# Performance work log

Measured on AMD Instinct MI355X. Metric: run time of the kernel, lower is better.

## Reference

```python
import jax, jax.numpy as jnp
import numpy as np

N_USERS = 100_000
N_ITEMS = 200_000
N_EDGES = 1_000_000
D = 64        # in_size == every layer_size
L = 3         # number of NGCF layers
B = 4096      # BPR batch
SLOPE = 0.2   # LeakyReLU negative slope
EPS = 1e-12   # F.normalize eps


def setup_inputs() -> dict:
    key = jax.random.key(0)
    ks = jax.random.split(key, 11)
    s = 1.0 / np.sqrt(D)  # xavier-ish scale
    return dict(
        user_feat=jax.random.normal(ks[0], (N_USERS, D), jnp.float32) * s,
        item_feat=jax.random.normal(ks[1], (N_ITEMS, D), jnp.float32) * s,
        W1=jax.random.normal(ks[2], (L, D, D), jnp.float32) * s,
        b1=jnp.zeros((L, D), jnp.float32),
        W2=jax.random.normal(ks[3], (L, D, D), jnp.float32) * s,
        b2=jnp.zeros((L, D), jnp.float32),
        edge_src=jax.random.randint(ks[4], (N_EDGES,), 0, N_USERS),
        edge_dst=jax.random.randint(ks[5], (N_EDGES,), 0, N_ITEMS),
        users=jax.random.randint(ks[6], (B,), 0, N_USERS),
        pos_items=jax.random.randint(ks[7], (B,), 0, N_ITEMS),
        neg_items=jax.random.randint(ks[8], (B,), 0, N_ITEMS),
    )


def _act_norm(h):
    # LeakyReLU(0.2) -> (dropout=identity, eval) -> row-wise L2 normalize
    h = jax.nn.leaky_relu(h, SLOPE)
    n = jnp.linalg.norm(h, axis=1, keepdims=True)
    return h / jnp.maximum(n, EPS)


def _ngcf_forward(user_feat, item_feat, W1, b1, W2, b2, edge_src, edge_dst):
    ones = jnp.ones((edge_src.shape[0],), user_feat.dtype)
    deg_u = jax.ops.segment_sum(ones, edge_src, num_segments=N_USERS)  # out-degree of users
    deg_i = jax.ops.segment_sum(ones, edge_dst, num_segments=N_ITEMS)  # in-degree of items
    norm = (deg_u[edge_src] * deg_i[edge_dst]) ** -0.5  # [E], same for both directions
    norm = norm[:, None]

    hu, hi = user_feat, item_feat
    u_embeds, i_embeds = [hu], [hi]
    for l in range(L):
        # per-edge elementwise product term (shared between both directions)
        p = hu[edge_src] * hi[edge_dst]            # [E, D]
        pw = p @ W2[l] + b2[l]                     # [E, D]
        # user -> item messages, summed per item
        m_i = norm * ((hu @ W1[l] + b1[l])[edge_src] + pw)
        # item -> user messages, summed per user
        m_u = norm * ((hi @ W1[l] + b1[l])[edge_dst] + pw)
        hi_new = jax.ops.segment_sum(m_i, edge_dst, num_segments=N_ITEMS)
        hu_new = jax.ops.segment_sum(m_u, edge_src, num_segments=N_USERS)
        hu, hi = _act_norm(hu_new), _act_norm(hi_new)
        u_embeds.append(hu)
        i_embeds.append(hi)

    user_embd = jnp.concatenate(u_embeds, axis=1)  # [N_USERS, D*(L+1)]
    item_embd = jnp.concatenate(i_embeds, axis=1)  # [N_ITEMS, D*(L+1)]
    return user_embd, item_embd


def reference(user_feat, item_feat, W1, b1, W2, b2,
              edge_src, edge_dst, users, pos_items, neg_items):
    user_embd, item_embd = _ngcf_forward(
        user_feat, item_feat, W1, b1, W2, b2, edge_src, edge_dst)
    return (user_embd[users], item_embd[pos_items], item_embd[neg_items])
```

## Files before the change

kernel.cpp:

```cpp
#include <hip/hip_runtime.h>

#define NU 100000
#define NI 200000
#define NE 1000000
#define NB 4096
#define CAP 16384
#define NBS 98
#define NBD 98
#define NTI (NI / 16)
#define NTU (NU / 16)

typedef __attribute__((ext_vector_type(8))) short bf16x8;
typedef __attribute__((ext_vector_type(4))) float f32x4;
typedef __attribute__((ext_vector_type(8))) unsigned short u16x8;

static __device__ __forceinline__ short f2bf(float f) {
  unsigned u = __builtin_bit_cast(unsigned, f);
  unsigned r = (u + 0x7fffu + ((u >> 16) & 1u)) >> 16;
  return (short)r;
}
static __device__ __forceinline__ float bf2f(unsigned short u) {
  return __builtin_bit_cast(float, ((unsigned)u) << 16);
}

__global__ __launch_bounds__(256) void binA_kernel(const int* __restrict__ src,
                                                   const int* __restrict__ dst,
                                                   int* __restrict__ gcur_s,
                                                   int* __restrict__ gcur_d,
                                                   int2* __restrict__ temp_s,
                                                   int2* __restrict__ temp_d) {
  __shared__ int lh[128], lbase[128], lpos[128];
  const int dir = blockIdx.x >> 9;
  const int cb = blockIdx.x & 511;
  const int lo = (int)(((long long)NE * cb) >> 9);
  const int hi = (int)(((long long)NE * (cb + 1)) >> 9);
  const int* key = dir ? dst : src;
  const int* oth = dir ? src : dst;
  int* gcur = dir ? gcur_d : gcur_s;
  int2* temp = dir ? temp_d : temp_s;
  const int shift = dir ? 11 : 10;
  const int tid = threadIdx.x;
  if (tid < 128) lh[tid] = 0;
  __syncthreads();
  for (int e = lo + tid; e < hi; e += 256) atomicAdd(&lh[key[e] >> shift], 1);
  __syncthreads();
  if (tid < 128) {
    const int c = lh[tid];
    lbase[tid] = c ? atomicAdd(&gcur[tid], c) : 0;
    lpos[tid] = 0;
  }
  __syncthreads();
  for (int e = lo + tid; e < hi; e += 256) {
    const int k = key[e];
    const int b = k >> shift;
    const int p = lbase[b] + atomicAdd(&lpos[b], 1);
    temp[(size_t)b * CAP + p] = make_int2(k, oth[e]);
  }
}

__global__ void bktscan_kernel(const int* __restrict__ gcur_s, const int* __restrict__ gcur_d,
                               int* __restrict__ bktofs_s, int* __restrict__ bktofs_d,
                               int* __restrict__ ofs_u, int* __restrict__ ofs_i) {
  const int t = threadIdx.x;
  if (t == 0) {
    int a = 0;
    for (int i = 0; i < NBS; ++i) { bktofs_s[i] = a; a += gcur_s[i]; }
    bktofs_s[NBS] = a;
    ofs_u[NU] = NE;
  }
  if (t == 1) {
    int a = 0;
    for (int i = 0; i < NBD; ++i) { bktofs_d[i] = a; a += gcur_d[i]; }
    bktofs_d[NBD] = a;
    ofs_i[NI] = NE;
  }
}

__global__ __launch_bounds__(256) void placeB_kernel(const int2* __restrict__ temp_s,
                                                     const int2* __restrict__ temp_d,
                                                     const int* __restrict__ gcur_s,
                                                     const int* __restrict__ gcur_d,
                                                     const int* __restrict__ bktofs_s,
                                                     const int* __restrict__ bktofs_d,
                                                     int* __restrict__ ofs_u, int* __restrict__ ofs_i,
                                                     float* __restrict__ rs_u, float* __restrict__ rs_i,
                                                     int* __restrict__ by_src, int* __restrict__ by_dst) {
  __shared__ int cnt[2048];
  __shared__ int exc[2048];
  __shared__ int wsum[256];
  const bool isdst = blockIdx.x >= NBS;
  const int b = isdst ? (int)blockIdx.x - NBS : (int)blockIdx.x;
  const int shift = isdst ? 11 : 10;
  const int nodelo = b << shift;
  const int n = isdst ? NI : NU;
  const int2* temp = (isdst ? temp_d : temp_s) + (size_t)b * CAP;
  const int ecnt = (isdst ? gcur_d : gcur_s)[b];
  const int bbase = (isdst ? bktofs_d : bktofs_s)[b];
  int* ofs = isdst ? ofs_i : ofs_u;
  float* rs = isdst ? rs_i : rs_u;
  int* by = isdst ? by_dst : by_src;
  const int tid = threadIdx.x;
  const int NN = 1 << shift;

  for (int j = tid; j < NN; j += 256) cnt[j] = 0;
  __syncthreads();
  for (int k = tid; k < ecnt; k += 256) atomicAdd(&cnt[temp[k].x - nodelo], 1);
  __syncthreads();
  const int per = NN >> 8;
  int s = 0;
  for (int j = 0; j < per; ++j) s += cnt[tid * per + j];
  wsum[tid] = s;
  __syncthreads();
  for (int off = 1; off < 256; off <<= 1) {
    int t2 = (tid >= off) ? wsum[tid - off] : 0;
    __syncthreads();
    wsum[tid] += t2;
    __syncthreads();
  }
  int run = wsum[tid] - s;
  for (int j = 0; j < per; ++j) {
    const int idx = tid * per + j;
    exc[idx] = run;
    run += cnt[idx];
  }
  __syncthreads();
  for (int j = tid; j < NN; j += 256) {
    const int node = nodelo + j;
    if (node < n) {
      ofs[node] = bbase + exc[j];
      const int d = cnt[j];
      rs[node] = d > 0 ? rsqrtf((float)d) : 0.f;
    }
  }
  __syncthreads();
  for (int j = tid; j < NN; j += 256) cnt[j] = exc[j];
  __syncthreads();
  for (int k = tid; k < ecnt; k += 256) {
    const int2 t2 = temp[k];
    const int p = bbase + atomicAdd(&cnt[t2.x - nodelo], 1);
    by[p] = t2.y;
  }
}

__global__ __launch_bounds__(256) void conv_kernel(const float* __restrict__ uf,
                                                   const float* __restrict__ itf,
                                                   unsigned short* __restrict__ hu,
                                                   unsigned short* __restrict__ hi) {
  int i = blockIdx.x * 256 + threadIdx.x;
  const int n4u = NU * 16;
  const float* in;
  unsigned short* outp;
  int j;
  if (i < n4u) {
    in = uf; outp = hu; j = i;
  } else if (i < n4u + NI * 16) {
    in = itf; outp = hi; j = i - n4u;
  } else return;
  float4 v = *(const float4*)&in[(size_t)j * 4];
  ushort4 o;
  o.x = (unsigned short)f2bf(v.x);
  o.y = (unsigned short)f2bf(v.y);
  o.z = (unsigned short)f2bf(v.z);
  o.w = (unsigned short)f2bf(v.w);
  *(ushort4*)&outp[(size_t)j * 4] = o;
}

__global__ __launch_bounds__(256) void gatherg_kernel(const int* __restrict__ ofs_i,
                                                      const int* __restrict__ ofs_u,
                                                      const int* __restrict__ by_dst,
                                                      const int* __restrict__ by_src,
                                                      const float* __restrict__ rs_u,
                                                      const float* __restrict__ rs_i,
                                                      const unsigned short* __restrict__ hu,
                                                      const unsigned short* __restrict__ hi,
                                                      unsigned short* __restrict__ g_i,
                                                      unsigned short* __restrict__ g_u,
                                                      float* __restrict__ c_i,
                                                      float* __restrict__ c_u) {
  const int lane = threadIdx.x & 63;
  const int w = threadIdx.x >> 6;
  const int j8 = lane & 7, grp = lane >> 3;
  const int r = blockIdx.x * 4 + w;
  if (r >= NI + NU) return;
  const bool item = r < NI;
  const int rr = item ? r : r - NI;
  const int* ofs = item ? ofs_i : ofs_u;
  const int* pay = item ? by_dst : by_src;
  const float* rso = item ? rs_u : rs_i;
  const float* rsw = item ? rs_i : rs_u;
  const unsigned short* hsrc = item ? hu : hi;
  unsigned short* g = item ? g_i : g_u;
  float* c = item ? c_i : c_u;

  const int lo = ofs[rr], hiE = ofs[rr + 1];
  float acc[8] = {0.f, 0.f, 0.f, 0.f, 0.f, 0.f, 0.f, 0.f};
  float cs = 0.f;
  for (int k = lo + grp; k < hiE; k += 8) {
    const int nb = pay[k];
    const float ww = rso[nb];
    const u16x8 hv = *(const u16x8*)(hsrc + (size_t)nb * 64 + j8 * 8);
#pragma unroll
    for (int j = 0; j < 8; ++j) acc[j] += ww * bf2f(hv[j]);
    cs += ww;
  }
#pragma unroll
  for (int m = 8; m < 64; m <<= 1) {
#pragma unroll
    for (int j = 0; j < 8; ++j) acc[j] += __shfl_xor(acc[j], m);
    cs += __shfl_xor(cs, m);
  }
  if (grp == 0) {
    const float rsn = rsw[rr];
    u16x8 o;
#pragma unroll
    for (int j = 0; j < 8; ++j) o[j] = (unsigned short)f2bf(acc[j] * rsn);
    *(u16x8*)(g + (size_t)rr * 64 + j8 * 8) = o;
    if (j8 == 0) c[rr] = cs * rsn;
  }
}

__global__ __launch_bounds__(256) void node_mfma_kernel(const unsigned short* __restrict__ g_i,
                                                        const unsigned short* __restrict__ g_u,
                                                        const float* __restrict__ c_i,
                                                        const float* __restrict__ c_u,
                                                        const unsigned short* __restrict__ hi,
                                                        const unsigned short* __restrict__ hu,
                                                        const float* __restrict__ W1,
                                                        const float* __restrict__ b1,
                                                        const float* __restrict__ W2,
                                                        const float* __restrict__ b2,
                                                        unsigned short* __restrict__ hi_new,
                                                        unsigned short* __restrict__ hu_new) {
  const int lane = threadIdx.x & 63;
  const int row16 = lane & 15;
  const int kgrp = lane >> 4;
  const int wid = (blockIdx.x * 256 + threadIdx.x) >> 6;
  const int nwaves = (gridDim.x * 256) >> 6;

  bf16x8 w1f[4][2], w2f[4][2];
#pragma unroll
  for (int nb = 0; nb < 4; ++nb)
#pragma unroll
    for (int kb = 0; kb < 2; ++kb) {
      const int n = nb * 16 + row16;
      const int k0 = kb * 32 + kgrp * 8;
      bf16x8 t1, t2;
#pragma unroll
      for (int j = 0; j < 8; ++j) {
        t1[j] = f2bf(W1[(k0 + j) * 64 + n]);
        t2[j] = f2bf(W2[(k0 + j) * 64 + n]);
      }
      w1f[nb][kb] = t1;
      w2f[nb][kb] = t2;
    }
  float bsum[4];
#pragma unroll
  for (int nb = 0; nb < 4; ++nb) bsum[nb] = b1[nb * 16 + row16] + b2[nb * 16 + row16];

  for (int t = wid; t < NTI + NTU; t += nwaves) {
    const bool item = t < NTI;
    const int tt = item ? t : t - NTI;
    const unsigned short* g = item ? g_i : g_u;
    const float* c = item ? c_i : c_u;
    const unsigned short* hold = item ? hi : hu;
    unsigned short* hnew = item ? hi_new : hu_new;
    const int r0 = tt * 16;

    const unsigned short* gp = g + (size_t)(r0 + row16) * 64 + kgrp * 8;
    const unsigned short* hp = hold + (size_t)(r0 + row16) * 64 + kgrp * 8;
    bf16x8 ag[2], ap[2];
#pragma unroll
    for (int kb = 0; kb < 2; ++kb) {
      const u16x8 gv = *(const u16x8*)(gp + kb * 32);
      const u16x8 hv = *(const u16x8*)(hp + kb * 32);
      ag[kb] = __builtin_bit_cast(bf16x8, gv);
      bf16x8 p;
#pragma unroll
      for (int j = 0; j < 8; ++j) p[j] = f2bf(bf2f(gv[j]) * bf2f(hv[j]));
      ap[kb] = p;
    }
    f32x4 acc[4];
#pragma unroll
    for (int nb = 0; nb < 4; ++nb) acc[nb] = (f32x4){0.f, 0.f, 0.f, 0.f};
#pragma unroll
    for (int nb = 0; nb < 4; ++nb)
#pragma unroll
      for (int kb = 0; kb < 2; ++kb) {
        acc[nb] = __builtin_amdgcn_mfma_f32_16x16x32_bf16(ag[kb], w1f[nb][kb], acc[nb], 0, 0, 0);
        acc[nb] = __builtin_amdgcn_mfma_f32_16x16x32_bf16(ap[kb], w2f[nb][kb], acc[nb], 0, 0, 0);
      }
    float cv[4];
#pragma unroll
    for (int reg = 0; reg < 4; ++reg) cv[reg] = c[r0 + kgrp * 4 + reg];
    float v[4][4];
    float ss[4] = {0.f, 0.f, 0.f, 0.f};
#pragma unroll
    for (int nb = 0; nb < 4; ++nb)
#pragma unroll
      for (int reg = 0; reg < 4; ++reg) {
        float x = acc[nb][reg] + cv[reg] * bsum[nb];
        x = (x > 0.f) ? x : 0.2f * x;
        v[nb][reg] = x;
        ss[reg] += x * x;
      }
#pragma unroll
    for (int m = 1; m < 16; m <<= 1)
#pragma unroll
      for (int reg = 0; reg < 4; ++reg) ss[reg] += __shfl_xor(ss[reg], m);
    float inv[4];
#pragma unroll
    for (int reg = 0; reg < 4; ++reg) inv[reg] = 1.0f / fmaxf(sqrtf(ss[reg]), 1e-12f);
#pragma unroll
    for (int reg = 0; reg < 4; ++reg) {
      const size_t rowbase = (size_t)(r0 + kgrp * 4 + reg) * 64;
#pragma unroll
      for (int nb = 0; nb < 4; ++nb)
        hnew[rowbase + nb * 16 + row16] = (unsigned short)f2bf(v[nb][reg] * inv[reg]);
    }
  }
}

__global__ __launch_bounds__(256) void gather_f32_kernel(const float* __restrict__ hu,
                                                         const float* __restrict__ hi,
                                                         const int* __restrict__ users,
                                                         const int* __restrict__ pos,
                                                         const int* __restrict__ neg,
                                                         float* __restrict__ out) {
  int t = blockIdx.x * 256 + threadIdx.x;
  if (t >= 3 * NB * 64) return;
  int j = t & 63;
  int b = (t >> 6) & (NB - 1);
  int which = t / (NB * 64);
  int row = (which == 0) ? users[b] : ((which == 1) ? pos[b] : neg[b]);
  const float* h = (which == 0) ? hu : hi;
  out[(size_t)which * NB * 256 + (size_t)b * 256 + j] = h[(size_t)row * 64 + j];
}

__global__ __launch_bounds__(256) void gather_bf_kernel(const unsigned short* __restrict__ hu,
                                                        const unsigned short* __restrict__ hi,
                                                        const int* __restrict__ users,
                                                        const int* __restrict__ pos,
                                                        const int* __restrict__ neg,
                                                        float* __restrict__ out, int stage) {
  int t = blockIdx.x * 256 + threadIdx.x;
  if (t >= 3 * NB * 64) return;
  int j = t & 63;
  int b = (t >> 6) & (NB - 1);
  int which = t / (NB * 64);
  int row = (which == 0) ? users[b] : ((which == 1) ? pos[b] : neg[b]);
  const unsigned short* h = (which == 0) ? hu : hi;
  out[(size_t)which * NB * 256 + (size_t)b * 256 + (size_t)stage * 64 + j] =
      bf2f(h[(size_t)row * 64 + j]);
}

extern "C" void kernel_launch(void* const* d_in, const int* in_sizes, int n_in,
                              void* d_out, int out_size, void* d_ws, size_t ws_size,
                              hipStream_t stream) {
  (void)in_sizes; (void)n_in; (void)out_size; (void)ws_size;
  const float* user_feat = (const float*)d_in[0];
  const float* item_feat = (const float*)d_in[1];
  const float* W1 = (const float*)d_in[2];
  const float* b1 = (const float*)d_in[3];
  const float* W2 = (const float*)d_in[4];
  const float* b2 = (const float*)d_in[5];
  const int* edge_src = (const int*)d_in[6];
  const int* edge_dst = (const int*)d_in[7];
  const int* users = (const int*)d_in[8];
  const int* pos_items = (const int*)d_in[9];
  const int* neg_items = (const int*)d_in[10];
  float* out = (float*)d_out;

  char* base = (char*)d_ws;
  size_t ofsz = 0;
  auto alloc = [&](size_t bytes) -> char* {
    char* r = base + ofsz;
    ofsz += (bytes + 1023) & ~(size_t)1023;
    return r;
  };
  int* ofs_u = (int*)alloc((NU + 1) * 4);
  int* ofs_i = (int*)alloc((NI + 1) * 4);
  int* gcur_s = (int*)alloc(128 * 4);
  int* gcur_d = (int*)alloc(128 * 4);
  int* bktofs_s = (int*)alloc(128 * 4);
  int* bktofs_d = (int*)alloc(128 * 4);
  int2* temp_s = (int2*)alloc((size_t)NBS * CAP * 8);
  int2* temp_d = (int2*)alloc((size_t)NBD * CAP * 8);
  int* by_src = (int*)alloc((size_t)NE * 4);
  int* by_dst = (int*)alloc((size_t)NE * 4);
  float* rs_u = (float*)alloc((size_t)NU * 4);
  float* rs_i = (float*)alloc((size_t)NI * 4);
  float* c_u = (float*)alloc((size_t)NU * 4);
  float* c_i = (float*)alloc((size_t)NI * 4);
  unsigned short* g_u = (unsigned short*)alloc((size_t)NU * 64 * 2);
  unsigned short* g_i = (unsigned short*)alloc((size_t)NI * 64 * 2);
  unsigned short* hbU0 = (unsigned short*)alloc((size_t)NU * 64 * 2);
  unsigned short* hbU1 = (unsigned short*)alloc((size_t)NU * 64 * 2);
  unsigned short* hbI0 = (unsigned short*)alloc((size_t)NI * 64 * 2);
  unsigned short* hbI1 = (unsigned short*)alloc((size_t)NI * 64 * 2);

  unsigned short* bufU[2] = {hbU1, hbU0};
  unsigned short* bufI[2] = {hbI1, hbI0};

  hipMemsetAsync(gcur_s, 0, 128 * 4, stream);
  hipMemsetAsync(gcur_d, 0, 128 * 4, stream);
  binA_kernel<<<1024, 256, 0, stream>>>(edge_src, edge_dst, gcur_s, gcur_d, temp_s, temp_d);
  bktscan_kernel<<<1, 64, 0, stream>>>(gcur_s, gcur_d, bktofs_s, bktofs_d, ofs_u, ofs_i);
  placeB_kernel<<<NBS + NBD, 256, 0, stream>>>(temp_s, temp_d, gcur_s, gcur_d,
                                               bktofs_s, bktofs_d, ofs_u, ofs_i,
                                               rs_u, rs_i, by_src, by_dst);

  conv_kernel<<<((NU + NI) * 16 + 255) / 256, 256, 0, stream>>>(user_feat, item_feat, hbU0, hbI0);

  gather_f32_kernel<<<(3 * NB * 64 + 255) / 256, 256, 0, stream>>>(
      user_feat, item_feat, users, pos_items, neg_items, out);

  const unsigned short* hu = hbU0;
  const unsigned short* hi = hbI0;
  for (int l = 0; l < 3; ++l) {
    unsigned short* hu_new = bufU[l & 1];
    unsigned short* hi_new = bufI[l & 1];
    gatherg_kernel<<<(NI + NU + 3) / 4, 256, 0, stream>>>(ofs_i, ofs_u, by_dst, by_src,
                                                          rs_u, rs_i, hu, hi, g_i, g_u, c_i, c_u);
    node_mfma_kernel<<<1024, 256, 0, stream>>>(g_i, g_u, c_i, c_u, hi, hu,
                                               W1 + l * 4096, b1 + l * 64,
                                               W2 + l * 4096, b2 + l * 64, hi_new, hu_new);
    gather_bf_kernel<<<(3 * NB * 64 + 255) / 256, 256, 0, stream>>>(
        hu_new, hi_new, users, pos_items, neg_items, out, l + 1);
    hu = hu_new;
    hi = hi_new;
  }
}
```

Baseline: 505.4 us.

## Fuse neighbor aggregation into per-tile MFMA node kernel

Merges the CSR neighbor-gather kernel into the MFMA node-update kernel. Each wave now aggregates neighbors for its 16-row tile directly in registers, with each lane handling one node and a quarter of its features, then feeds the MFMA. This removes the intermediate g and c buffers and one launch per layer. The cost is that each lane walks its node's edge list serially, so divergence from uneven degrees within a tile may reduce memory parallelism compared with the previous 8-way per-node edge split.

Result: faster. 426.9 us (-15.5%).

```diff
diff --git a/kernel.cpp b/kernel.cpp
--- a/kernel.cpp
+++ b/kernel.cpp
@@ -165,75 +165,23 @@
   *(ushort4*)&outp[(size_t)j * 4] = o;
 }
 
-__global__ __launch_bounds__(256) void gatherg_kernel(const int* __restrict__ ofs_i,
-                                                      const int* __restrict__ ofs_u,
-                                                      const int* __restrict__ by_dst,
-                                                      const int* __restrict__ by_src,
-                                                      const float* __restrict__ rs_u,
-                                                      const float* __restrict__ rs_i,
-                                                      const unsigned short* __restrict__ hu,
-                                                      const unsigned short* __restrict__ hi,
-                                                      unsigned short* __restrict__ g_i,
-                                                      unsigned short* __restrict__ g_u,
-                                                      float* __restrict__ c_i,
-                                                      float* __restrict__ c_u) {
-  const int lane = threadIdx.x & 63;
-  const int w = threadIdx.x >> 6;
-  const int j8 = lane & 7, grp = lane >> 3;
-  const int r = blockIdx.x * 4 + w;
-  if (r >= NI + NU) return;
-  const bool item = r < NI;
-  const int rr = item ? r : r - NI;
-  const int* ofs = item ? ofs_i : ofs_u;
-  const int* pay = item ? by_dst : by_src;
-  const float* rso = item ? rs_u : rs_i;
-  const float* rsw = item ? rs_i : rs_u;
-  const unsigned short* hsrc = item ? hu : hi;
-  unsigned short* g = item ? g_i : g_u;
-  float* c = item ? c_i : c_u;
-
-  const int lo = ofs[rr], hiE = ofs[rr + 1];
-  float acc[8] = {0.f, 0.f, 0.f, 0.f, 0.f, 0.f, 0.f, 0.f};
-  float cs = 0.f;
-  for (int k = lo + grp; k < hiE; k += 8) {
-    const int nb = pay[k];
-    const float ww = rso[nb];
-    const u16x8 hv = *(const u16x8*)(hsrc + (size_t)nb * 64 + j8 * 8);
-#pragma unroll
-    for (int j = 0; j < 8; ++j) acc[j] += ww * bf2f(hv[j]);
-    cs += ww;
-  }
-#pragma unroll
-  for (int m = 8; m < 64; m <<= 1) {
-#pragma unroll
-    for (int j = 0; j < 8; ++j) acc[j] += __shfl_xor(acc[j], m);
-    cs += __shfl_xor(cs, m);
-  }
-  if (grp == 0) {
-    const float rsn = rsw[rr];
-    u16x8 o;
-#pragma unroll
-    for (int j = 0; j < 8; ++j) o[j] = (unsigned short)f2bf(acc[j] * rsn);
-    *(u16x8*)(g + (size_t)rr * 64 + j8 * 8) = o;
-    if (j8 == 0) c[rr] = cs * rsn;
-  }
-}
-
-__global__ __launch_bounds__(256) void node_mfma_kernel(const unsigned short* __restrict__ g_i,
-                                                        const unsigned short* __restrict__ g_u,
-                                                        const float* __restrict__ c_i,
-                                                        const float* __restrict__ c_u,
-                                                        const unsigned short* __restrict__ hi,
-                                                        const unsigned short* __restrict__ hu,
-                                                        const float* __restrict__ W1,
-                                                        const float* __restrict__ b1,
-                                                        const float* __restrict__ W2,
-                                                        const float* __restrict__ b2,
-                                                        unsigned short* __restrict__ hi_new,
-                                                        unsigned short* __restrict__ hu_new) {
+__global__ __launch_bounds__(256) void layer_fused_kernel(const int* __restrict__ ofs_i,
+                                                          const int* __restrict__ ofs_u,
+                                                          const int* __restrict__ by_dst,
+                                                          const int* __restrict__ by_src,
+                                                          const float* __restrict__ rs_u,
+                                                          const float* __restrict__ rs_i,
+                                                          const unsigned short* __restrict__ hu,
+                                                          const unsigned short* __restrict__ hi,
+                                                          const float* __restrict__ W1,
+                                                          const float* __restrict__ b1,
+                                                          const float* __restrict__ W2,
+                                                          const float* __restrict__ b2,
+                                                          unsigned short* __restrict__ hi_new,
+                                                          unsigned short* __restrict__ hu_new) {
   const int lane = threadIdx.x & 63;
   const int row16 = lane & 15;
-  const int kgrp = lane >> 4;
+  const int kg = lane >> 4;
   const int wid = (blockIdx.x * 256 + threadIdx.x) >> 6;
   const int nwaves = (gridDim.x * 256) >> 6;
 
@@ -243,7 +191,7 @@
 #pragma unroll
     for (int kb = 0; kb < 2; ++kb) {
       const int n = nb * 16 + row16;
-      const int k0 = kb * 32 + kgrp * 8;
+      const int k0 = kb * 32 + kg * 8;
       bf16x8 t1, t2;
 #pragma unroll
       for (int j = 0; j < 8; ++j) {
@@ -260,25 +208,51 @@
   for (int t = wid; t < NTI + NTU; t += nwaves) {
     const bool item = t < NTI;
     const int tt = item ? t : t - NTI;
-    const unsigned short* g = item ? g_i : g_u;
-    const float* c = item ? c_i : c_u;
+    const int* ofs = item ? ofs_i : ofs_u;
+    const int* pay = item ? by_dst : by_src;
+    const float* rso = item ? rs_u : rs_i;
+    const float* rsw = item ? rs_i : rs_u;
+    const unsigned short* hsrc = item ? hu : hi;
     const unsigned short* hold = item ? hi : hu;
     unsigned short* hnew = item ? hi_new : hu_new;
     const int r0 = tt * 16;
-
-    const unsigned short* gp = g + (size_t)(r0 + row16) * 64 + kgrp * 8;
-    const unsigned short* hp = hold + (size_t)(r0 + row16) * 64 + kgrp * 8;
+    const int node = r0 + row16;
+
+    const int lo = ofs[node], hiE = ofs[node + 1];
+    float a0[8] = {0.f, 0.f, 0.f, 0.f, 0.f, 0.f, 0.f, 0.f};
+    float a1[8] = {0.f, 0.f, 0.f, 0.f, 0.f, 0.f, 0.f, 0.f};
+    float cs = 0.f;
+    for (int i = lo;; ++i) {
+      const bool act = i < hiE;
+      if (!__any(act)) break;
+      if (act) {
+        const int nb = pay[i];
+        const float ww = rso[nb];
+        const u16x8 h0 = *(const u16x8*)(hsrc + (size_t)nb * 64 + kg * 8);
+        const u16x8 h1 = *(const u16x8*)(hsrc + (size_t)nb * 64 + kg * 8 + 32);
+#pragma unroll
+        for (int j = 0; j < 8; ++j) {
+          a0[j] += ww * bf2f(h0[j]);
+          a1[j] += ww * bf2f(h1[j]);
+        }
+        cs += ww;
+      }
+    }
+    const float rsn = rsw[node];
+    const u16x8 hv0 = *(const u16x8*)(hold + (size_t)node * 64 + kg * 8);
+    const u16x8 hv1 = *(const u16x8*)(hold + (size_t)node * 64 + kg * 8 + 32);
     bf16x8 ag[2], ap[2];
 #pragma unroll
-    for (int kb = 0; kb < 2; ++kb) {
-      const u16x8 gv = *(const u16x8*)(gp + kb * 32);
-      const u16x8 hv = *(const u16x8*)(hp + kb * 32);
-      ag[kb] = __builtin_bit_cast(bf16x8, gv);
-      bf16x8 p;
-#pragma unroll
-      for (int j = 0; j < 8; ++j) p[j] = f2bf(bf2f(gv[j]) * bf2f(hv[j]));
-      ap[kb] = p;
+    for (int j = 0; j < 8; ++j) {
+      const float g0 = a0[j] * rsn;
+      const float g1 = a1[j] * rsn;
+      ag[0][j] = f2bf(g0);
+      ag[1][j] = f2bf(g1);
+      ap[0][j] = f2bf(g0 * bf2f(hv0[j]));
+      ap[1][j] = f2bf(g1 * bf2f(hv1[j]));
     }
+    const float csc = cs * rsn;
+
     f32x4 acc[4];
 #pragma unroll
     for (int nb = 0; nb < 4; ++nb) acc[nb] = (f32x4){0.f, 0.f, 0.f, 0.f};
@@ -291,7 +265,7 @@
       }
     float cv[4];
 #pragma unroll
-    for (int reg = 0; reg < 4; ++reg) cv[reg] = c[r0 + kgrp * 4 + reg];
+    for (int reg = 0; reg < 4; ++reg) cv[reg] = __shfl(csc, kg * 4 + reg);
     float v[4][4];
     float ss[4] = {0.f, 0.f, 0.f, 0.f};
 #pragma unroll
@@ -312,7 +286,7 @@
     for (int reg = 0; reg < 4; ++reg) inv[reg] = 1.0f / fmaxf(sqrtf(ss[reg]), 1e-12f);
 #pragma unroll
     for (int reg = 0; reg < 4; ++reg) {
-      const size_t rowbase = (size_t)(r0 + kgrp * 4 + reg) * 64;
+      const size_t rowbase = (size_t)(r0 + kg * 4 + reg) * 64;
 #pragma unroll
       for (int nb = 0; nb < 4; ++nb)
         hnew[rowbase + nb * 16 + row16] = (unsigned short)f2bf(v[nb][reg] * inv[reg]);
@@ -389,10 +363,6 @@
   int* by_dst = (int*)alloc((size_t)NE * 4);
   float* rs_u = (float*)alloc((size_t)NU * 4);
   float* rs_i = (float*)alloc((size_t)NI * 4);
-  float* c_u = (float*)alloc((size_t)NU * 4);
-  float* c_i = (float*)alloc((size_t)NI * 4);
-  unsigned short* g_u = (unsigned short*)alloc((size_t)NU * 64 * 2);
-  unsigned short* g_i = (unsigned short*)alloc((size_t)NI * 64 * 2);
   unsigned short* hbU0 = (unsigned short*)alloc((size_t)NU * 64 * 2);
   unsigned short* hbU1 = (unsigned short*)alloc((size_t)NU * 64 * 2);
   unsigned short* hbI0 = (unsigned short*)alloc((size_t)NI * 64 * 2);
@@ -419,11 +389,11 @@
   for (int l = 0; l < 3; ++l) {
     unsigned short* hu_new = bufU[l & 1];
     unsigned short* hi_new = bufI[l & 1];
-    gatherg_kernel<<<(NI + NU + 3) / 4, 256, 0, stream>>>(ofs_i, ofs_u, by_dst, by_src,
-                                                          rs_u, rs_i, hu, hi, g_i, g_u, c_i, c_u);
-    node_mfma_kernel<<<1024, 256, 0, stream>>>(g_i, g_u, c_i, c_u, hi, hu,
-                                               W1 + l * 4096, b1 + l * 64,
-                                               W2 + l * 4096, b2 + l * 64, hi_new, hu_new);
+    layer_fused_kernel<<<1024, 256, 0, stream>>>(ofs_i, ofs_u, by_dst, by_src,
+                                                 rs_u, rs_i, hu, hi,
+                                                 W1 + l * 4096, b1 + l * 64,
+                                                 W2 + l * 4096, b2 + l * 64,
+                                                 hi_new, hu_new);
     gather_bf_kernel<<<(3 * NB * 64 + 255) / 256, 256, 0, stream>>>(
         hu_new, hi_new, users, pos_items, neg_items, out, l + 1);
     hu = hu_new;
```
